# Kernel tuning notes

Measured on AMD Instinct MI355X. Metric: run time of the kernel, lower is better.

The kernel has to match this reference:

```python
import jax, jax.numpy as jnp
import numpy as np


def setup_inputs() -> dict:
    key = jax.random.key(0)
    ks = jax.random.split(key, 11)
    B, S, D = 2, 2048, 1024
    s = 0.02
    return {
        "query": jax.random.normal(ks[0], (B, S, D), jnp.float32),
        "key": jax.random.normal(ks[1], (B, S, D), jnp.float32),
        "value": jax.random.normal(ks[2], (B, S, D), jnp.float32),
        "Wq": jax.random.normal(ks[3], (D, D), jnp.float32) * s,
        "bq": jnp.zeros((D,), jnp.float32),
        "Wk": jax.random.normal(ks[4], (D, D), jnp.float32) * s,
        "bk": jnp.zeros((D,), jnp.float32),
        "Wv": jax.random.normal(ks[5], (D, D), jnp.float32) * s,
        "bv": jnp.zeros((D,), jnp.float32),
        "Wo": jax.random.normal(ks[6], (D, D), jnp.float32) * s,
        "bo": jnp.zeros((D,), jnp.float32),
        "nheads": 16,
    }


def reference(query, key, value, Wq, bq, Wk, bk, Wv, bv, Wo, bo, nheads):
    B, Sq, D = query.shape
    Sk = key.shape[1]
    hd = D // nheads  # head dim
    q = (query @ Wq.T + bq).reshape(B, Sq, nheads, hd)
    k = (key @ Wk.T + bk).reshape(B, Sk, nheads, hd)
    v = (value @ Wv.T + bv).reshape(B, Sk, nheads, hd)
    score = jnp.einsum("bqhd,bkhd->bhqk", q, k)
    # mask == 'triu': strictly-upper-triangular entries set to -inf (causal)
    causal = jnp.triu(jnp.ones((Sq, Sk), dtype=bool), k=1)
    score = jnp.where(causal, -jnp.inf, score)
    # NOTE: original scales by sqrt(score.shape[-1]) == sqrt(kv_len), not sqrt(head_dim)
    scale = np.float32(1.0 / np.sqrt(Sk))
    att = jax.nn.softmax(score * scale, axis=-1)
    ret = jnp.einsum("bhqk,bkhd->bqhd", att, v).reshape(B, Sq, D)
    out = ret @ Wo.T + bo  # dropout is identity in eval mode
    return (out, att)
```

## Files before the change

### kernel.cpp

```cpp
#include <hip/hip_runtime.h>
#include <cstdint>
#include <cstddef>
#include <type_traits>

typedef __attribute__((ext_vector_type(8))) __bf16 bf16x8;
typedef __attribute__((ext_vector_type(4))) __bf16 bf16x4;
typedef __attribute__((ext_vector_type(4))) float f32x4;
typedef __attribute__((ext_vector_type(4))) unsigned short u16x4;

__device__ __forceinline__ f32x4 mfma16(bf16x8 a, bf16x8 b, f32x4 c) {
  return __builtin_amdgcn_mfma_f32_16x16x32_bf16(a, b, c, 0, 0, 0);
}

__device__ __forceinline__ void load_lds16(const void* g, void* l) {
  auto gp = reinterpret_cast<const __attribute__((address_space(1))) uint32_t*>(
      reinterpret_cast<uintptr_t>(g));
  auto lp = reinterpret_cast<__attribute__((address_space(3))) uint32_t*>(
      static_cast<uint32_t>(reinterpret_cast<uintptr_t>(l)));
  __builtin_amdgcn_global_load_lds(gp, lp, 16, 0, 0);
}

static constexpr float QPRE = 0.03187935710091218f;

static constexpr size_t OFF_XQ = 0;
static constexpr size_t OFF_XK = 4194304;
static constexpr size_t OFF_XV = 8388608;
static constexpr size_t OFF_WQ = 12582912;
static constexpr size_t OFF_WK = 13631488;
static constexpr size_t OFF_WV = 14680064;
static constexpr size_t OFF_WO = 15728640;
static constexpr size_t OFF_QB = 16777216;
static constexpr size_t OFF_KB = 20971520;
static constexpr size_t OFF_VT = 25165824;
static constexpr size_t OFF_RT = 29360128;

__global__ __launch_bounds__(256) void convert_all(
    const float* __restrict__ q, const float* __restrict__ k,
    const float* __restrict__ v, const float* __restrict__ wq,
    const float* __restrict__ wk, const float* __restrict__ wv,
    const float* __restrict__ wo, __bf16* __restrict__ ws)
{
  const int total = 2097152;
  for (int i = blockIdx.x * blockDim.x + threadIdx.x; i < total;
       i += gridDim.x * blockDim.x) {
    const float* src; size_t dstoff; int rel;
    if (i < 1572864) {
      if (i < 524288)       { src = q;  dstoff = OFF_XQ; rel = i; }
      else if (i < 1048576) { src = k;  dstoff = OFF_XK; rel = i - 524288; }
      else                  { src = v;  dstoff = OFF_XV; rel = i - 1048576; }
    } else if (i < 1835008) {
      if (i < 1703936)      { src = wq; dstoff = OFF_WQ; rel = i - 1572864; }
      else                  { src = wk; dstoff = OFF_WK; rel = i - 1703936; }
    } else if (i < 1966080) { src = wv; dstoff = OFF_WV; rel = i - 1835008; }
    else                    { src = wo; dstoff = OFF_WO; rel = i - 1966080; }
    float4 f0 = reinterpret_cast<const float4*>(src)[(size_t)rel * 2];
    float4 f1 = reinterpret_cast<const float4*>(src)[(size_t)rel * 2 + 1];
    bf16x8 o;
    o[0] = (__bf16)f0.x; o[1] = (__bf16)f0.y; o[2] = (__bf16)f0.z; o[3] = (__bf16)f0.w;
    o[4] = (__bf16)f1.x; o[5] = (__bf16)f1.y; o[6] = (__bf16)f1.z; o[7] = (__bf16)f1.w;
    *reinterpret_cast<bf16x8*>(ws + dstoff + (size_t)rel * 8) = o;
  }
}

__device__ __forceinline__ void gemm_body(
    const __bf16* __restrict__ A, const __bf16* __restrict__ Bm,
    const float* __restrict__ bias, void* __restrict__ Cout,
    int M, int N, int K, int mode, int m0, int n0,
    __bf16* As, __bf16* Bs)
{
  const int t = threadIdx.x;
  const int lane = t & 63, r = lane & 15, g = lane >> 4;
  const int w = t >> 6, wm = w >> 1, wn = w & 1;
  const int srow = t >> 3, scol = (t & 7) * 8;

  const f32x4 fzero = {0.f, 0.f, 0.f, 0.f};
  f32x4 acc[4][4];
#pragma unroll
  for (int x = 0; x < 4; x++)
#pragma unroll
    for (int y = 0; y < 4; y++) acc[x][y] = fzero;

  auto stage = [&](int buf, int k0) {
#pragma unroll
    for (int i = 0; i < 4; i++) {
      load_lds16(A  + (size_t)(m0 + i * 32 + srow) * K + k0 + scol, &As[buf * 8192 + i * 2048 + t * 8]);
      load_lds16(Bm + (size_t)(n0 + i * 32 + srow) * K + k0 + scol, &Bs[buf * 8192 + i * 2048 + t * 8]);
    }
  };

  const int NT = K / 64;
  stage(0, 0);
  asm volatile("s_waitcnt vmcnt(0)" ::: "memory");
  __syncthreads();
  int cur = 0;
  for (int kt = 0; kt < NT; ++kt) {
    if (kt + 1 < NT) stage(cur ^ 1, (kt + 1) * 64);
    const __bf16* Ab = &As[cur * 8192];
    const __bf16* Bb = &Bs[cur * 8192];
#pragma unroll
    for (int kk = 0; kk < 2; kk++) {
      bf16x8 af[4], bfv[4];
#pragma unroll
      for (int x = 0; x < 4; x++)
        af[x] = *reinterpret_cast<const bf16x8*>(&Ab[(wm * 64 + x * 16 + r) * 64 + kk * 32 + g * 8]);
#pragma unroll
      for (int y = 0; y < 4; y++)
        bfv[y] = *reinterpret_cast<const bf16x8*>(&Bb[(wn * 64 + y * 16 + r) * 64 + kk * 32 + g * 8]);
#pragma unroll
      for (int x = 0; x < 4; x++)
#pragma unroll
        for (int y = 0; y < 4; y++)
          acc[x][y] = mfma16(af[x], bfv[y], acc[x][y]);
    }
    asm volatile("s_waitcnt vmcnt(0)" ::: "memory");
    __syncthreads();
    cur ^= 1;
  }

#pragma unroll
  for (int x = 0; x < 4; x++)
#pragma unroll
    for (int y = 0; y < 4; y++) {
#pragma unroll
      for (int j = 0; j < 4; j++) {
        int row = m0 + wm * 64 + x * 16 + g * 4 + j;
        int col = n0 + wn * 64 + y * 16 + r;
        float val = acc[x][y][j];
        if (mode == 0 || mode == 1) {
          val += bias[col];
          if (mode == 0) val *= QPRE;
          int b = row >> 11, s = row & 2047, h = col >> 6, d = col & 63;
          ((__bf16*)Cout)[(((size_t)(b * 16 + h) * 2048 + s) << 6) + d] = (__bf16)val;
        } else if (mode == 2) {
          val += bias[row];
          int h = row >> 6, d = row & 63, b = col >> 11, s = col & 2047;
          ((__bf16*)Cout)[(((size_t)(b * 16 + h) * 64 + d) << 11) + s] = (__bf16)val;
        } else {
          val += bias[col];
          __builtin_nontemporal_store(val, &((float*)Cout)[(size_t)row * N + col]);
        }
      }
    }
}

__global__ __launch_bounds__(256) void gemm_qkv(
    __bf16* __restrict__ ws, const float* __restrict__ bq,
    const float* __restrict__ bk, const float* __restrict__ bv)
{
  __shared__ __align__(16) __bf16 As[2 * 8192];
  __shared__ __align__(16) __bf16 Bs[2 * 8192];
  const int z = blockIdx.z;
  if (z == 0) {
    gemm_body(ws + OFF_XQ, ws + OFF_WQ, bq, ws + OFF_QB, 4096, 1024, 1024, 0,
              blockIdx.y * 128, blockIdx.x * 128, As, Bs);
  } else if (z == 1) {
    gemm_body(ws + OFF_XK, ws + OFF_WK, bk, ws + OFF_KB, 4096, 1024, 1024, 1,
              blockIdx.y * 128, blockIdx.x * 128, As, Bs);
  } else {
    gemm_body(ws + OFF_WV, ws + OFF_XV, bv, ws + OFF_VT, 1024, 4096, 1024, 2,
              blockIdx.x * 128, blockIdx.y * 128, As, Bs);
  }
}

__global__ __launch_bounds__(256) void gemm_o(
    const __bf16* __restrict__ Rt, const __bf16* __restrict__ Wo,
    const float* __restrict__ bo, float* __restrict__ out)
{
  __shared__ __align__(16) __bf16 As[2 * 8192];
  __shared__ __align__(16) __bf16 Bs[2 * 8192];
  gemm_body(Rt, Wo, bo, out, 4096, 1024, 1024, 3,
            blockIdx.y * 128, blockIdx.x * 128, As, Bs);
}

__global__ __launch_bounds__(512) void attn_kernel(
    const __bf16* __restrict__ Qb, const __bf16* __restrict__ Kb,
    const __bf16* __restrict__ Vt, __bf16* __restrict__ Rt,
    float* __restrict__ att)
{
  __shared__ __align__(16) __bf16 Ks[128 * 68];
  __shared__ __align__(16) __bf16 Vts[64 * 132];
  __shared__ __align__(16) __bf16 Ps[128 * 132];

  const int t = threadIdx.x;
  const int lane = t & 63, r = lane & 15, g = lane >> 4;
  const int w = t >> 6;
  const int p = blockIdx.x;
  const int workid = (p & 7) * 64 + (p >> 3);
  const int bh = workid >> 4;
  const int xx = workid & 15;
  const int qb = ((bh >> 1) & 1) ? 15 - xx : xx;
  const int q0 = qb * 128;
  const __bf16* Qg = Qb + (size_t)bh * 2048 * 64;
  const __bf16* Kg = Kb + (size_t)bh * 2048 * 64;
  const __bf16* Vg = Vt + (size_t)bh * 64 * 2048;
  float* attb = att + (size_t)bh * 2048 * 2048 + (size_t)q0 * 2048;

  const int lrow = t >> 3, lcol = (t & 7) * 8;
  const int vrow = t >> 4, vcol = (t & 15) * 8;

  const f32x4 fzero = {0.f, 0.f, 0.f, 0.f};

  bf16x8 aq[2];
#pragma unroll
  for (int kk = 0; kk < 2; kk++)
    aq[kk] = *reinterpret_cast<const bf16x8*>(
        Qg + (size_t)(q0 + w * 16 + r) * 64 + kk * 32 + g * 8);

  auto compute_scores = [&](f32x4(&accs)[8]) {
#pragma unroll
    for (int nf = 0; nf < 8; nf++) accs[nf] = fzero;
    __builtin_amdgcn_s_setprio(1);
#pragma unroll
    for (int kk = 0; kk < 2; kk++) {
#pragma unroll
      for (int nf = 0; nf < 8; nf++) {
        bf16x8 bk = *reinterpret_cast<const bf16x8*>(&Ks[(nf * 16 + r) * 68 + kk * 32 + g * 8]);
        accs[nf] = mfma16(aq[kk], bk, accs[nf]);
      }
    }
    __builtin_amdgcn_s_setprio(0);
  };

  float rsp[4];
#pragma unroll
  for (int j = 0; j < 4; j++) rsp[j] = 0.f;

  bf16x8 rk[2];
#pragma unroll
  for (int i = 0; i < 2; i++)
    rk[i] = *reinterpret_cast<const bf16x8*>(Kg + (size_t)(i * 64 + lrow) * 64 + lcol);

  for (int kt = 0; kt <= qb; ++kt) {
    __syncthreads();
#pragma unroll
    for (int i = 0; i < 2; i++)
      *reinterpret_cast<bf16x8*>(&Ks[(i * 64 + lrow) * 68 + lcol]) = rk[i];
    __syncthreads();
    if (kt < qb) {
#pragma unroll
      for (int i = 0; i < 2; i++)
        rk[i] = *reinterpret_cast<const bf16x8*>(Kg + (size_t)((kt + 1) * 128 + i * 64 + lrow) * 64 + lcol);
    }
    f32x4 accs[8];
    compute_scores(accs);

    auto p1body = [&](auto maskc) {
      constexpr bool MASK = decltype(maskc)::value;
#pragma unroll
      for (int nf = 0; nf < 8; nf++) {
        int col = kt * 128 + nf * 16 + r;
#pragma unroll
        for (int j = 0; j < 4; j++) {
          float e = __builtin_amdgcn_exp2f(accs[nf][j]);
          if (MASK) {
            int rowg = q0 + w * 16 + g * 4 + j;
            e = (col <= rowg) ? e : 0.f;
          }
          rsp[j] += e;
        }
      }
    };
    if (kt == qb) p1body(std::integral_constant<bool, true>{});
    else          p1body(std::integral_constant<bool, false>{});
  }

  float rl[4];
#pragma unroll
  for (int j = 0; j < 4; j++) {
    float v2 = rsp[j];
    v2 += __shfl_xor(v2, 1, 64);
    v2 += __shfl_xor(v2, 2, 64);
    v2 += __shfl_xor(v2, 4, 64);
    v2 += __shfl_xor(v2, 8, 64);
    rl[j] = 1.0f / v2;
  }

  f32x4 accr[4];
#pragma unroll
  for (int nf2 = 0; nf2 < 4; nf2++) accr[nf2] = fzero;

  bf16x8 rv[2];
#pragma unroll
  for (int i = 0; i < 2; i++) {
    rk[i] = *reinterpret_cast<const bf16x8*>(Kg + (size_t)(i * 64 + lrow) * 64 + lcol);
    rv[i] = *reinterpret_cast<const bf16x8*>(Vg + (size_t)(i * 32 + vrow) * 2048 + vcol);
  }

  for (int kt = 0; kt <= qb; ++kt) {
    __syncthreads();
#pragma unroll
    for (int i = 0; i < 2; i++) {
      *reinterpret_cast<bf16x8*>(&Ks[(i * 64 + lrow) * 68 + lcol]) = rk[i];
      *reinterpret_cast<bf16x8*>(&Vts[(i * 32 + vrow) * 132 + vcol]) = rv[i];
    }
    __syncthreads();
    if (kt < qb) {
#pragma unroll
      for (int i = 0; i < 2; i++) {
        rk[i] = *reinterpret_cast<const bf16x8*>(Kg + (size_t)((kt + 1) * 128 + i * 64 + lrow) * 64 + lcol);
        rv[i] = *reinterpret_cast<const bf16x8*>(Vg + (size_t)(i * 32 + vrow) * 2048 + (kt + 1) * 128 + vcol);
      }
    }
    f32x4 accs[8];
    compute_scores(accs);

    auto p2body = [&](auto maskc) {
      constexpr bool MASK = decltype(maskc)::value;
#pragma unroll
      for (int nf = 0; nf < 8; nf++) {
        int col = kt * 128 + nf * 16 + r;
#pragma unroll
        for (int j = 0; j < 4; j++) {
          int rowl = w * 16 + g * 4 + j;
          float e = __builtin_amdgcn_exp2f(accs[nf][j]);
          if (MASK) {
            e = (col <= q0 + rowl) ? e : 0.f;
          }
          float pp = e * rl[j];
          Ps[rowl * 132 + nf * 16 + r] = (__bf16)pp;
        }
      }
    };
    if (kt == qb) p2body(std::integral_constant<bool, true>{});
    else          p2body(std::integral_constant<bool, false>{});

    __syncthreads();
    __builtin_amdgcn_s_setprio(1);
#pragma unroll
    for (int kk2 = 0; kk2 < 4; kk2++) {
      bf16x8 ap = *reinterpret_cast<const bf16x8*>(&Ps[(w * 16 + r) * 132 + kk2 * 32 + g * 8]);
#pragma unroll
      for (int nf2 = 0; nf2 < 4; nf2++) {
        bf16x8 bv_ = *reinterpret_cast<const bf16x8*>(&Vts[(nf2 * 16 + r) * 132 + kk2 * 32 + g * 8]);
        accr[nf2] = mfma16(ap, bv_, accr[nf2]);
      }
    }
    __builtin_amdgcn_s_setprio(0);

    {
      const int half = lane >> 5;
      const int c4 = lane & 31;
#pragma unroll
      for (int j = 0; j < 8; j++) {
        int rowl = w * 16 + 2 * j + half;
        u16x4 pv = *reinterpret_cast<const u16x4*>(&Ps[rowl * 132 + c4 * 4]);
        f32x4 f;
        f[0] = __uint_as_float((unsigned)pv[0] << 16);
        f[1] = __uint_as_float((unsigned)pv[1] << 16);
        f[2] = __uint_as_float((unsigned)pv[2] << 16);
        f[3] = __uint_as_float((unsigned)pv[3] << 16);
        __builtin_nontemporal_store(
            f, reinterpret_cast<f32x4*>(attb + (size_t)rowl * 2048 + kt * 128 + c4 * 4));
      }
    }
  }

  const f32x4 z4 = {0.f, 0.f, 0.f, 0.f};
  for (int kt2 = qb + 1; kt2 < 16; ++kt2) {
    for (int idx = t; idx < 4096; idx += 512) {
      int row = idx >> 5, c4 = idx & 31;
      __builtin_nontemporal_store(
          z4, reinterpret_cast<f32x4*>(attb + (size_t)row * 2048 + kt2 * 128 + c4 * 4));
    }
  }

  const int b = bh >> 4, h = bh & 15;
#pragma unroll
  for (int nf2 = 0; nf2 < 4; nf2++)
#pragma unroll
    for (int j = 0; j < 4; j++) {
      int qrow = q0 + w * 16 + g * 4 + j;
      int d = nf2 * 16 + r;
      Rt[((size_t)(b * 2048 + qrow) << 10) + h * 64 + d] = (__bf16)accr[nf2][j];
    }
}

extern "C" void kernel_launch(void* const* d_in, const int* in_sizes, int n_in,
                              void* d_out, int out_size, void* d_ws, size_t ws_size,
                              hipStream_t stream) {
  (void)in_sizes; (void)n_in; (void)out_size; (void)ws_size;
  const float* q  = (const float*)d_in[0];
  const float* k  = (const float*)d_in[1];
  const float* v  = (const float*)d_in[2];
  const float* wq = (const float*)d_in[3];
  const float* bq = (const float*)d_in[4];
  const float* wk = (const float*)d_in[5];
  const float* bk = (const float*)d_in[6];
  const float* wv = (const float*)d_in[7];
  const float* bv = (const float*)d_in[8];
  const float* wo = (const float*)d_in[9];
  const float* bo = (const float*)d_in[10];
  __bf16* ws = (__bf16*)d_ws;
  float* out = (float*)d_out;
  float* att = out + 4194304;

  convert_all<<<2048, 256, 0, stream>>>(q, k, v, wq, wk, wv, wo, ws);
  gemm_qkv<<<dim3(8, 32, 3), 256, 0, stream>>>(ws, bq, bk, bv);
  attn_kernel<<<512, 512, 0, stream>>>(ws + OFF_QB, ws + OFF_KB, ws + OFF_VT, ws + OFF_RT, att);
  gemm_o<<<dim3(8, 32), 256, 0, stream>>>(ws + OFF_RT, ws + OFF_WO, bo, out);
}
```

Before: 201.4 us.

## Double-buffer K tiles in the softmax-sum pass and drop a redundant barrier

The first attention pass (row-sum of exponentials) now alternates between two shared-memory K buffers, with the second buffer aliased onto the V tile region. This needs one block barrier per K tile instead of two. In the second pass, the barrier between writing the probability tile and the P·V MFMAs is removed, since each wave reads back only the rows it wrote itself. The trade-off is that the global K load is now written to shared memory right after it is issued, rather than overlapping with the score computation. That may expose load latency.

```diff
diff --git a/kernel.cpp b/kernel.cpp
--- a/kernel.cpp
+++ b/kernel.cpp
@@ -177,9 +177,11 @@
     const __bf16* __restrict__ Vt, __bf16* __restrict__ Rt,
     float* __restrict__ att)
 {
-  __shared__ __align__(16) __bf16 Ks[128 * 68];
-  __shared__ __align__(16) __bf16 Vts[64 * 132];
-  __shared__ __align__(16) __bf16 Ps[128 * 132];
+  __shared__ __align__(16) __bf16 smem[34048];
+  __bf16* const KsA = smem;
+  __bf16* const KsB = smem + 8704;
+  __bf16* const Vts = smem + 8704;
+  __bf16* const Ps  = smem + 17152;
 
   const int t = threadIdx.x;
   const int lane = t & 63, r = lane & 15, g = lane >> 4;
@@ -206,7 +208,7 @@
     aq[kk] = *reinterpret_cast<const bf16x8*>(
         Qg + (size_t)(q0 + w * 16 + r) * 64 + kk * 32 + g * 8);
 
-  auto compute_scores = [&](f32x4(&accs)[8]) {
+  auto compute_scores = [&](const __bf16* Kl, f32x4(&accs)[8]) {
 #pragma unroll
     for (int nf = 0; nf < 8; nf++) accs[nf] = fzero;
     __builtin_amdgcn_s_setprio(1);
@@ -214,54 +216,74 @@
     for (int kk = 0; kk < 2; kk++) {
 #pragma unroll
       for (int nf = 0; nf < 8; nf++) {
-        bf16x8 bk = *reinterpret_cast<const bf16x8*>(&Ks[(nf * 16 + r) * 68 + kk * 32 + g * 8]);
+        bf16x8 bk = *reinterpret_cast<const bf16x8*>(&Kl[(nf * 16 + r) * 68 + kk * 32 + g * 8]);
         accs[nf] = mfma16(aq[kk], bk, accs[nf]);
       }
     }
     __builtin_amdgcn_s_setprio(0);
   };
 
+  bf16x8 rk[2];
+  auto loadK = [&](int kt2) {
+#pragma unroll
+    for (int i = 0; i < 2; i++)
+      rk[i] = *reinterpret_cast<const bf16x8*>(Kg + (size_t)(kt2 * 128 + i * 64 + lrow) * 64 + lcol);
+  };
+  auto writeKto = [&](__bf16* dst) {
+#pragma unroll
+    for (int i = 0; i < 2; i++)
+      *reinterpret_cast<bf16x8*>(&dst[(i * 64 + lrow) * 68 + lcol]) = rk[i];
+  };
+
   float rsp[4];
 #pragma unroll
   for (int j = 0; j < 4; j++) rsp[j] = 0.f;
 
-  bf16x8 rk[2];
-#pragma unroll
-  for (int i = 0; i < 2; i++)
-    rk[i] = *reinterpret_cast<const bf16x8*>(Kg + (size_t)(i * 64 + lrow) * 64 + lcol);
-
-  for (int kt = 0; kt <= qb; ++kt) {
-    __syncthreads();
-#pragma unroll
-    for (int i = 0; i < 2; i++)
-      *reinterpret_cast<bf16x8*>(&Ks[(i * 64 + lrow) * 68 + lcol]) = rk[i];
-    __syncthreads();
-    if (kt < qb) {
-#pragma unroll
-      for (int i = 0; i < 2; i++)
-        rk[i] = *reinterpret_cast<const bf16x8*>(Kg + (size_t)((kt + 1) * 128 + i * 64 + lrow) * 64 + lcol);
-    }
-    f32x4 accs[8];
-    compute_scores(accs);
-
-    auto p1body = [&](auto maskc) {
-      constexpr bool MASK = decltype(maskc)::value;
-#pragma unroll
-      for (int nf = 0; nf < 8; nf++) {
-        int col = kt * 128 + nf * 16 + r;
-#pragma unroll
-        for (int j = 0; j < 4; j++) {
-          float e = __builtin_amdgcn_exp2f(accs[nf][j]);
-          if (MASK) {
-            int rowg = q0 + w * 16 + g * 4 + j;
-            e = (col <= rowg) ? e : 0.f;
-          }
-          rsp[j] += e;
+  auto p1body = [&](f32x4(&accs)[8], int kt, auto maskc) {
+    constexpr bool MASK = decltype(maskc)::value;
+#pragma unroll
+    for (int nf = 0; nf < 8; nf++) {
+      int col = kt * 128 + nf * 16 + r;
+#pragma unroll
+      for (int j = 0; j < 4; j++) {
+        float e = __builtin_amdgcn_exp2f(accs[nf][j]);
+        if (MASK) {
+          int rowg = q0 + w * 16 + g * 4 + j;
+          e = (col <= rowg) ? e : 0.f;
         }
-      }
-    };
-    if (kt == qb) p1body(std::integral_constant<bool, true>{});
-    else          p1body(std::integral_constant<bool, false>{});
+        rsp[j] += e;
+      }
+    }
+  };
+  auto p1tile = [&](f32x4(&accs)[8], int kt) {
+    if (kt == qb) p1body(accs, kt, std::integral_constant<bool, true>{});
+    else          p1body(accs, kt, std::integral_constant<bool, false>{});
+  };
+
+  loadK(0);
+  writeKto(KsA);
+  {
+    int kt = 0;
+    while (kt + 1 <= qb) {
+      __syncthreads();
+      loadK(kt + 1);
+      writeKto(KsB);
+      f32x4 accsA[8];
+      compute_scores(KsA, accsA);
+      p1tile(accsA, kt);
+      __syncthreads();
+      if (kt + 2 <= qb) { loadK(kt + 2); writeKto(KsA); }
+      f32x4 accsB[8];
+      compute_scores(KsB, accsB);
+      p1tile(accsB, kt + 1);
+      kt += 2;
+    }
+    if (kt <= qb) {
+      __syncthreads();
+      f32x4 accsA[8];
+      compute_scores(KsA, accsA);
+      p1tile(accsA, kt);
+    }
   }
 
   float rl[4];
@@ -280,29 +302,27 @@
   for (int nf2 = 0; nf2 < 4; nf2++) accr[nf2] = fzero;
 
   bf16x8 rv[2];
-#pragma unroll
-  for (int i = 0; i < 2; i++) {
-    rk[i] = *reinterpret_cast<const bf16x8*>(Kg + (size_t)(i * 64 + lrow) * 64 + lcol);
+  loadK(0);
+#pragma unroll
+  for (int i = 0; i < 2; i++)
     rv[i] = *reinterpret_cast<const bf16x8*>(Vg + (size_t)(i * 32 + vrow) * 2048 + vcol);
-  }
 
   for (int kt = 0; kt <= qb; ++kt) {
     __syncthreads();
 #pragma unroll
     for (int i = 0; i < 2; i++) {
-      *reinterpret_cast<bf16x8*>(&Ks[(i * 64 + lrow) * 68 + lcol]) = rk[i];
+      *reinterpret_cast<bf16x8*>(&KsA[(i * 64 + lrow) * 68 + lcol]) = rk[i];
       *reinterpret_cast<bf16x8*>(&Vts[(i * 32 + vrow) * 132 + vcol]) = rv[i];
     }
     __syncthreads();
     if (kt < qb) {
-#pragma unroll
-      for (int i = 0; i < 2; i++) {
-        rk[i] = *reinterpret_cast<const bf16x8*>(Kg + (size_t)((kt + 1) * 128 + i * 64 + lrow) * 64 + lcol);
+      loadK(kt + 1);
+#pragma unroll
+      for (int i = 0; i < 2; i++)
         rv[i] = *reinterpret_cast<const bf16x8*>(Vg + (size_t)(i * 32 + vrow) * 2048 + (kt + 1) * 128 + vcol);
-      }
     }
     f32x4 accs[8];
-    compute_scores(accs);
+    compute_scores(KsA, accs);
 
     auto p2body = [&](auto maskc) {
       constexpr bool MASK = decltype(maskc)::value;
@@ -324,7 +344,6 @@
     if (kt == qb) p2body(std::integral_constant<bool, true>{});
     else          p2body(std::integral_constant<bool, false>{});
 
-    __syncthreads();
     __builtin_amdgcn_s_setprio(1);
 #pragma unroll
     for (int kk2 = 0; kk2 < 4; kk2++) {
```

After: 413.4 us. 105% more time.
